# Kernel optimization log

Hardware: AMD Instinct MI355X
Metric: run time of the kernel (lower is better)

Reference implementation:

```python
import jax, jax.numpy as jnp
import numpy as np

RADIUS = 1.0
NSAMPLE = 32


def setup_inputs() -> dict:
    key = jax.random.key(0)
    k1, k2, k3, k4, k5 = jax.random.split(key, 5)
    B, Nb, M, K, C = 2, 2048, 64, 216, 32
    N = B * Nb
    # points in a 20m cube
    xyz = jax.random.uniform(k1, (N, 3), dtype=jnp.float32) * 20.0
    xyz_batch_cnt = jnp.array([Nb, Nb], dtype=jnp.int32)
    # rois: [x,y,z,dx,dy,dz,ry]
    ctr = jax.random.uniform(k2, (B, M, 3), dtype=jnp.float32) * 20.0
    dims = 1.0 + jax.random.uniform(k3, (B, M, 3), dtype=jnp.float32) * 2.0
    ry = jax.random.uniform(k4, (B, M, 1), dtype=jnp.float32) * 6.28
    rois = jnp.concatenate([ctr, dims, ry], axis=-1)
    # 6x6x6 grid points jittered around each roi center
    off = (jax.random.uniform(k5, (B, M, K, 3), dtype=jnp.float32) - 0.5) * 3.0
    new_xyz = ctr[:, :, None, :] + off
    features = jax.random.normal(jax.random.fold_in(key, 7), (N, C), dtype=jnp.float32)
    return {"xyz": xyz, "xyz_batch_cnt": xyz_batch_cnt, "new_xyz": new_xyz,
            "rois": rois, "features": features}


def _query_and_group(xyz, new_xyz, rois, features, B, Nb):
    """Ball query -> ragged compaction (padded to L=N*nsample) -> gather."""
    M, K = new_xyz.shape[1], new_xyz.shape[2]
    MK = M * K
    N = B * Nb
    L = N * NSAMPLE
    xyz_b = xyz.reshape(B, Nb, 3)
    grid = new_xyz.reshape(B, MK, 3)
    # squared distances point -> grid center, (B, Nb, MK)
    d2 = jnp.sum((xyz_b[:, :, None, :] - grid[:, None, :, :]) ** 2, axis=-1)
    # roi bounding sphere: center rois[:,:,:3], radius ||dims||_2 (the `ball` tensor)
    ctr = rois[:, :, :3]
    r2 = jnp.sum(rois[:, :, 3:6] ** 2, axis=-1)          # (B, M)
    d2b = jnp.sum((xyz_b[:, :, None, :] - ctr[:, None, :, :]) ** 2, axis=-1)  # (B,Nb,M)
    in_ball = (d2b <= r2[:, None, :])[:, :, :, None]      # (B,Nb,M,1)
    mask = (d2 <= RADIUS * RADIUS) & jnp.broadcast_to(in_ball, (B, Nb, M, K)).reshape(B, Nb, MK)
    # first-NSAMPLE-in-order selection per point (matches kernel iteration order)
    rank = jnp.cumsum(mask.astype(jnp.int32), axis=2) - 1
    cols = jnp.where(mask & (rank < NSAMPLE), rank, NSAMPLE)  # NSAMPLE = OOB -> dropped
    rows = jnp.broadcast_to(
        jnp.arange(B, dtype=jnp.int32)[:, None, None] * Nb
        + jnp.arange(Nb, dtype=jnp.int32)[None, :, None], (B, Nb, MK))
    flat_idx = jnp.broadcast_to(
        jnp.arange(B, dtype=jnp.int32)[:, None, None] * MK
        + jnp.arange(MK, dtype=jnp.int32)[None, None, :], (B, Nb, MK))
    ball_idx = jnp.full((N, NSAMPLE), -1, dtype=jnp.int32)
    ball_idx = ball_idx.at[rows.reshape(-1), cols.reshape(-1)].set(
        flat_idx.reshape(-1), mode="drop")
    # BallIndice: cumsum compaction of valid (point_idx, grid_idx) pairs, row-major
    valid = (ball_idx > -1).reshape(-1)                  # (L,)
    pos = jnp.cumsum(valid.astype(jnp.int32)) - 1
    pos_w = jnp.where(valid, pos, L)                     # invalid -> OOB -> dropped
    row_ids = jnp.broadcast_to(
        jnp.arange(N, dtype=jnp.int32)[:, None], (N, NSAMPLE)).reshape(-1)
    set_indices = jnp.zeros((L,), jnp.int32).at[pos_w].set(row_ids, mode="drop")
    set_new_indices = jnp.zeros((L,), jnp.int32).at[pos_w].set(
        ball_idx.reshape(-1), mode="drop")
    nind = jnp.sum(valid.astype(jnp.int32))
    vm = (jnp.arange(L) < nind)[:, None].astype(features.dtype)  # padding mask
    # GatherFeature (padded slots zeroed, matching new_zeros semantics)
    group_xyz = xyz[set_indices] * vm
    group_new_xyz = new_xyz.reshape(-1, 3)[set_new_indices] * vm
    group_feat = features[set_indices] * vm
    group_features = jnp.concatenate([group_xyz - group_new_xyz, group_feat], axis=1)
    return group_features, set_new_indices


def reference(xyz, xyz_batch_cnt, new_xyz, rois, features):
    B = xyz_batch_cnt.shape[0]
    Nb = xyz.shape[0] // B
    return _query_and_group(xyz, new_xyz, rois, features, B, Nb)
```

## Files before the change

### kernel.cpp

```cpp
#include <hip/hip_runtime.h>


#pragma clang fp contract(off)

typedef unsigned long long u64;

#define MAXN 4096

__global__ __launch_bounds__(256) void count_kernel(
    const float* __restrict__ xyz, const float* __restrict__ new_xyz,
    const float* __restrict__ rois, int* __restrict__ counts,
    int* __restrict__ blockSums, int* __restrict__ ballidx,
    int N, int Nb, int M, int K, int nsample)
{
    __shared__ int plist[4][64];
    __shared__ int scnt[4];
    const int wave = threadIdx.x >> 6;
    const int lane = threadIdx.x & 63;
    const int r = blockIdx.x * 4 + wave;
    const u64 laneLt = (1ull << lane) - 1ull;

    int cntc = 0;
    if (r < N) {
        const int b  = r / Nb;
        const float px = xyz[3 * r + 0];
        const float py = xyz[3 * r + 1];
        const float pz = xyz[3 * r + 2];

        bool pass = false;
        if (lane < M) {
            const float* rp = rois + (size_t)(b * M + lane) * 7;
            const float dx = rp[3], dy = rp[4], dz = rp[5];
            const float r2 = (dx * dx + dy * dy) + dz * dz;
            const float ex = px - rp[0], ey = py - rp[1], ez = pz - rp[2];
            pass = ((ex * ex + ey * ey) + ez * ez) <= r2;
        }
        const u64 roiMask = __ballot(pass);
        if (roiMask) {
            if (pass) plist[wave][__popcll(roiMask & laneLt)] = lane;

            const int P = __popcll(roiMask);
            const int total = P * K;
            const float* nb_ = new_xyz + (size_t)(b * M * K) * 3;
            int* bi = ballidx + (size_t)r * nsample;

            int cnt = 0;
            for (int base = 0; base < total && cnt < nsample; base += 512) {
                bool match[8];
                int jj[8];
                #pragma unroll
                for (int u = 0; u < 8; u++) {
                    const int p = base + u * 64 + lane;
                    match[u] = false; jj[u] = 0;
                    if (p < total) {
                        const int ri = p / K;
                        const int k  = p - ri * K;
                        const int j  = plist[wave][ri] * K + k;
                        jj[u] = j;
                        const float* gp = nb_ + (size_t)j * 3;
                        const float ax = px - gp[0], ay = py - gp[1], az = pz - gp[2];
                        match[u] = ((ax * ax + ay * ay) + az * az) <= 1.0f;
                    }
                }
                #pragma unroll
                for (int u = 0; u < 8; u++) {
                    const u64 mm = __ballot(match[u]);
                    const int slot = cnt + __popcll(mm & laneLt);
                    if (match[u] && slot < nsample) bi[slot] = jj[u];
                    cnt += __popcll(mm);
                }
            }
            cntc = cnt > nsample ? nsample : cnt;
        }
        if (lane == 0) counts[r] = cntc;
    }
    if (lane == 0) scnt[wave] = cntc;
    __syncthreads();
    if (threadIdx.x == 0)
        blockSums[blockIdx.x] = scnt[0] + scnt[1] + scnt[2] + scnt[3];
}

__global__ __launch_bounds__(256) void emit_kernel(
    const float* __restrict__ xyz, const float* __restrict__ new_xyz,
    const float* __restrict__ features,
    const int* __restrict__ counts, const int* __restrict__ blockSums,
    const int* __restrict__ ballidx,
    float* __restrict__ out_feat, float* __restrict__ out_idx,
    int N, int Nb, int M, int K, int C, int nsample, int numBlocks)
{
    __shared__ int sred[8];
    const int t = threadIdx.x;
    const int lane = t & 63;
    const int wid = t >> 6;
    const int bid = blockIdx.x;

    int pre = 0, tot = 0;
    {
        const int g = (t + bid) & 255;
        const int b0 = g * 4;
        #pragma unroll
        for (int i = 0; i < 4; i++) {
            const int bb = b0 + i;
            if (bb < numBlocks) {
                const int v = blockSums[bb];
                tot += v;
                if (bb < bid) pre += v;
            }
        }
        #pragma unroll
        for (int d = 1; d < 64; d <<= 1) {
            pre += __shfl_xor(pre, d, 64);
            tot += __shfl_xor(tot, d, 64);
        }
        if (lane == 0) { sred[wid] = pre; sred[4 + wid] = tot; }
    }
    __syncthreads();
    const int blockPre = sred[0] + sred[1] + sred[2] + sred[3];
    const int nind     = sred[4] + sred[5] + sred[6] + sred[7];

    const int W = 3 + C;
    const size_t L = (size_t)N * nsample;
    const int r0 = bid * 4;
    const int r  = r0 + wid;

    if (r < N) {
        const int cnt = counts[r];
        if (cnt > 0) {
            int rowpre = 0;
            if (lane < wid && (r0 + lane) < N) rowpre = counts[r0 + lane];
            #pragma unroll
            for (int d = 1; d < 64; d <<= 1) rowpre += __shfl_xor(rowpre, d, 64);

            const int b  = r / Nb;
            const int MK = M * K;
            const int obase = blockPre + rowpre;
            const int* bi = ballidx + (size_t)r * nsample;
            const float px = xyz[3 * r + 0];
            const float py = xyz[3 * r + 1];
            const float pz = xyz[3 * r + 2];
            const float* fr = features + (size_t)r * C;
            const float* nb_ = new_xyz + (size_t)b * MK * 3;

            float* dst = out_feat + (size_t)obase * W;
            const int totE = cnt * W;
            for (int idx = lane; idx < totE; idx += 64) {
                const int s = idx / W;
                const int c = idx - s * W;
                const int j = bi[s];
                float v;
                if (c == 0)      v = px - nb_[(size_t)j * 3 + 0];
                else if (c == 1) v = py - nb_[(size_t)j * 3 + 1];
                else if (c == 2) v = pz - nb_[(size_t)j * 3 + 2];
                else             v = fr[c - 3];
                dst[idx] = v;
            }
            for (int s = lane; s < cnt; s += 64)
                out_idx[obase + s] = (float)(b * MK + bi[s]);
        }
    }

    const int gtid = bid * 256 + t;
    const int gthreads = gridDim.x * 256;
    {
        const size_t sA = (size_t)nind * W;
        const size_t eA = L * (size_t)W;
        if (sA < eA) {
            const size_t s4 = (sA + 3) & ~(size_t)3;
            const size_t headEnd = s4 < eA ? s4 : eA;
            if ((size_t)gtid < headEnd - sA) out_feat[sA + gtid] = 0.0f;
            if (s4 < eA) {
                const size_t nvec = (eA - s4) >> 2;
                float4* p4 = (float4*)(out_feat + s4);
                const float4 z = make_float4(0.0f, 0.0f, 0.0f, 0.0f);
                for (size_t i = gtid; i < nvec; i += gthreads) p4[i] = z;
                const size_t rem = (eA - s4) & 3;
                if ((size_t)gtid < rem) out_feat[eA - rem + gtid] = 0.0f;
            }
        }
    }
    for (size_t i = (size_t)nind + gtid; i < L; i += gthreads)
        out_idx[i] = 0.0f;
}

extern "C" void kernel_launch(void* const* d_in, const int* in_sizes, int n_in,
                              void* d_out, int out_size, void* d_ws, size_t ws_size,
                              hipStream_t stream) {
    if (n_in < 5) return;

    int bc = 0;
    for (int i = 1; i < n_in; i++) if (in_sizes[i] < in_sizes[bc]) bc = i;
    const int B = in_sizes[bc];
    if (B < 1) return;

    int xi = -1, nwi = -1, ri = -1, fi = -1;
    int N = 0, M = 0, K = 0, C = 0, nsample = 0;

    for (int rr = 0; rr < n_in && xi < 0; rr++) {
        if (rr == bc) continue;
        if (in_sizes[rr] % (7 * B)) continue;
        const int M_ = in_sizes[rr] / (7 * B);
        if (M_ < 1 || M_ > 64) continue;
        for (int xx = 0; xx < n_in && xi < 0; xx++) {
            if (xx == bc || xx == rr) continue;
            if (in_sizes[xx] % 3) continue;
            const int N_ = in_sizes[xx] / 3;
            if (N_ < B || N_ % B || N_ > MAXN) continue;
            for (int nn = 0; nn < n_in && xi < 0; nn++) {
                if (nn == bc || nn == rr || nn == xx) continue;
                if (in_sizes[nn] % (3 * B * M_)) continue;
                const int K_ = in_sizes[nn] / (3 * B * M_);
                if (K_ < 1) continue;
                for (int ff = 0; ff < n_in && xi < 0; ff++) {
                    if (ff == bc || ff == rr || ff == xx || ff == nn) continue;
                    if (in_sizes[ff] % N_) continue;
                    const int C_ = in_sizes[ff] / N_;
                    if (C_ < 1) continue;
                    if (out_size % (4 + C_)) continue;
                    const long long L_ = (long long)out_size / (4 + C_);
                    if (L_ % N_) continue;
                    const int ns = (int)(L_ / N_);
                    if (ns < 1 || ns > 1024) continue;
                    xi = xx; nwi = nn; ri = rr; fi = ff;
                    N = N_; M = M_; K = K_; C = C_; nsample = ns;
                }
            }
        }
    }
    if (xi < 0) return;

    const float* xyz      = (const float*)d_in[xi];
    const float* new_xyz  = (const float*)d_in[nwi];
    const float* rois     = (const float*)d_in[ri];
    const float* features = (const float*)d_in[fi];
    const int Nb = N / B;

    const size_t L      = (size_t)N * nsample;
    const size_t chunk0 = L * (size_t)(3 + C);

    float* out_feat = (float*)d_out;
    float* out_idx  = out_feat + chunk0;

    const int blocks = (N + 3) / 4;

    const size_t wsNeed = ((size_t)N + (size_t)blocks + (size_t)N * nsample) * sizeof(int);
    if (ws_size < wsNeed) return;
    int* counts    = (int*)d_ws;
    int* blockSums = counts + N;
    int* ballidx   = blockSums + blocks;

    count_kernel<<<blocks, 256, 0, stream>>>(
        xyz, new_xyz, rois, counts, blockSums, ballidx,
        N, Nb, M, K, nsample);
    emit_kernel<<<blocks, 256, 0, stream>>>(
        xyz, new_xyz, features, counts, blockSums, ballidx,
        out_feat, out_idx, N, Nb, M, K, C, nsample, blocks);
}
```

Baseline: 88.35 us.

## Use 8 rows per block, 16-bit ball indices, nontemporal stores, per-wave prefix

Block size doubles to 512 threads with 8 rows per block, which halves the grid. Ball indices are stored as 16-bit values when M*K fits, shrinking the workspace traffic. Every output write, including the large zero-fill, now uses a nontemporal store to avoid cache pollution. The block prefix sum is computed redundantly in each wave over all block sums, dropping the shared-memory reduction and the barrier, but each wave now loops over more entries.

New measurement: 90.41 us. 1.02x slower.

```diff
diff --git a/kernel.cpp b/kernel.cpp
--- a/kernel.cpp
+++ b/kernel.cpp
@@ -4,20 +4,23 @@
 #pragma clang fp contract(off)
 
 typedef unsigned long long u64;
+typedef float f32x4 __attribute__((ext_vector_type(4)));
 
 #define MAXN 4096
-
-__global__ __launch_bounds__(256) void count_kernel(
+#define RPB 8
+
+template <typename IT>
+__global__ __launch_bounds__(512) void count_kernel(
     const float* __restrict__ xyz, const float* __restrict__ new_xyz,
     const float* __restrict__ rois, int* __restrict__ counts,
-    int* __restrict__ blockSums, int* __restrict__ ballidx,
+    int* __restrict__ blockSums, IT* __restrict__ ballidx,
     int N, int Nb, int M, int K, int nsample)
 {
-    __shared__ int plist[4][64];
-    __shared__ int scnt[4];
+    __shared__ int plist[RPB][64];
+    __shared__ int scnt[RPB];
     const int wave = threadIdx.x >> 6;
     const int lane = threadIdx.x & 63;
-    const int r = blockIdx.x * 4 + wave;
+    const int r = blockIdx.x * RPB + wave;
     const u64 laneLt = (1ull << lane) - 1ull;
 
     int cntc = 0;
@@ -42,7 +45,7 @@
             const int P = __popcll(roiMask);
             const int total = P * K;
             const float* nb_ = new_xyz + (size_t)(b * M * K) * 3;
-            int* bi = ballidx + (size_t)r * nsample;
+            IT* bi = ballidx + (size_t)r * nsample;
 
             int cnt = 0;
             for (int base = 0; base < total && cnt < nsample; base += 512) {
@@ -66,7 +69,7 @@
                 for (int u = 0; u < 8; u++) {
                     const u64 mm = __ballot(match[u]);
                     const int slot = cnt + __popcll(mm & laneLt);
-                    if (match[u] && slot < nsample) bi[slot] = jj[u];
+                    if (match[u] && slot < nsample) bi[slot] = (IT)jj[u];
                     cnt += __popcll(mm);
                 }
             }
@@ -76,19 +79,23 @@
     }
     if (lane == 0) scnt[wave] = cntc;
     __syncthreads();
-    if (threadIdx.x == 0)
-        blockSums[blockIdx.x] = scnt[0] + scnt[1] + scnt[2] + scnt[3];
+    if (threadIdx.x == 0) {
+        int s = 0;
+        #pragma unroll
+        for (int i = 0; i < RPB; i++) s += scnt[i];
+        blockSums[blockIdx.x] = s;
+    }
 }
 
-__global__ __launch_bounds__(256) void emit_kernel(
+template <typename IT>
+__global__ __launch_bounds__(512) void emit_kernel(
     const float* __restrict__ xyz, const float* __restrict__ new_xyz,
     const float* __restrict__ features,
     const int* __restrict__ counts, const int* __restrict__ blockSums,
-    const int* __restrict__ ballidx,
+    const IT* __restrict__ ballidx,
     float* __restrict__ out_feat, float* __restrict__ out_idx,
     int N, int Nb, int M, int K, int C, int nsample, int numBlocks)
 {
-    __shared__ int sred[8];
     const int t = threadIdx.x;
     const int lane = t & 63;
     const int wid = t >> 6;
@@ -96,31 +103,24 @@
 
     int pre = 0, tot = 0;
     {
-        const int g = (t + bid) & 255;
-        const int b0 = g * 4;
-        #pragma unroll
-        for (int i = 0; i < 4; i++) {
-            const int bb = b0 + i;
-            if (bb < numBlocks) {
-                const int v = blockSums[bb];
-                tot += v;
-                if (bb < bid) pre += v;
-            }
+        const int g = (lane + bid) & 63;
+        for (int idx = g; idx < numBlocks; idx += 64) {
+            const int v = blockSums[idx];
+            tot += v;
+            if (idx < bid) pre += v;
         }
         #pragma unroll
         for (int d = 1; d < 64; d <<= 1) {
             pre += __shfl_xor(pre, d, 64);
             tot += __shfl_xor(tot, d, 64);
         }
-        if (lane == 0) { sred[wid] = pre; sred[4 + wid] = tot; }
-    }
-    __syncthreads();
-    const int blockPre = sred[0] + sred[1] + sred[2] + sred[3];
-    const int nind     = sred[4] + sred[5] + sred[6] + sred[7];
+    }
+    const int blockPre = pre;
+    const int nind     = tot;
 
     const int W = 3 + C;
     const size_t L = (size_t)N * nsample;
-    const int r0 = bid * 4;
+    const int r0 = bid * RPB;
     const int r  = r0 + wid;
 
     if (r < N) {
@@ -134,7 +134,7 @@
             const int b  = r / Nb;
             const int MK = M * K;
             const int obase = blockPre + rowpre;
-            const int* bi = ballidx + (size_t)r * nsample;
+            const IT* bi = ballidx + (size_t)r * nsample;
             const float px = xyz[3 * r + 0];
             const float py = xyz[3 * r + 1];
             const float pz = xyz[3 * r + 2];
@@ -146,40 +146,44 @@
             for (int idx = lane; idx < totE; idx += 64) {
                 const int s = idx / W;
                 const int c = idx - s * W;
-                const int j = bi[s];
+                const int j = (int)bi[s];
                 float v;
                 if (c == 0)      v = px - nb_[(size_t)j * 3 + 0];
                 else if (c == 1) v = py - nb_[(size_t)j * 3 + 1];
                 else if (c == 2) v = pz - nb_[(size_t)j * 3 + 2];
                 else             v = fr[c - 3];
-                dst[idx] = v;
+                __builtin_nontemporal_store(v, &dst[idx]);
             }
             for (int s = lane; s < cnt; s += 64)
-                out_idx[obase + s] = (float)(b * MK + bi[s]);
-        }
-    }
-
-    const int gtid = bid * 256 + t;
-    const int gthreads = gridDim.x * 256;
+                __builtin_nontemporal_store((float)(b * MK + (int)bi[s]),
+                                            &out_idx[obase + s]);
+        }
+    }
+
+    const int gtid = bid * 512 + t;
+    const size_t gthreads = (size_t)numBlocks * 512;
     {
         const size_t sA = (size_t)nind * W;
         const size_t eA = L * (size_t)W;
         if (sA < eA) {
             const size_t s4 = (sA + 3) & ~(size_t)3;
             const size_t headEnd = s4 < eA ? s4 : eA;
-            if ((size_t)gtid < headEnd - sA) out_feat[sA + gtid] = 0.0f;
+            if ((size_t)gtid < headEnd - sA)
+                __builtin_nontemporal_store(0.0f, &out_feat[sA + gtid]);
             if (s4 < eA) {
                 const size_t nvec = (eA - s4) >> 2;
-                float4* p4 = (float4*)(out_feat + s4);
-                const float4 z = make_float4(0.0f, 0.0f, 0.0f, 0.0f);
-                for (size_t i = gtid; i < nvec; i += gthreads) p4[i] = z;
+                f32x4* p4 = (f32x4*)(out_feat + s4);
+                const f32x4 z = {0.0f, 0.0f, 0.0f, 0.0f};
+                for (size_t i = gtid; i < nvec; i += gthreads)
+                    __builtin_nontemporal_store(z, &p4[i]);
                 const size_t rem = (eA - s4) & 3;
-                if ((size_t)gtid < rem) out_feat[eA - rem + gtid] = 0.0f;
+                if ((size_t)gtid < rem)
+                    __builtin_nontemporal_store(0.0f, &out_feat[eA - rem + gtid]);
             }
         }
     }
     for (size_t i = (size_t)nind + gtid; i < L; i += gthreads)
-        out_idx[i] = 0.0f;
+        __builtin_nontemporal_store(0.0f, &out_idx[i]);
 }
 
 extern "C" void kernel_launch(void* const* d_in, const int* in_sizes, int n_in,
@@ -240,18 +244,29 @@
     float* out_feat = (float*)d_out;
     float* out_idx  = out_feat + chunk0;
 
-    const int blocks = (N + 3) / 4;
+    const int blocks = (N + RPB - 1) / RPB;
 
     const size_t wsNeed = ((size_t)N + (size_t)blocks + (size_t)N * nsample) * sizeof(int);
     if (ws_size < wsNeed) return;
     int* counts    = (int*)d_ws;
     int* blockSums = counts + N;
-    int* ballidx   = blockSums + blocks;
-
-    count_kernel<<<blocks, 256, 0, stream>>>(
-        xyz, new_xyz, rois, counts, blockSums, ballidx,
-        N, Nb, M, K, nsample);
-    emit_kernel<<<blocks, 256, 0, stream>>>(
-        xyz, new_xyz, features, counts, blockSums, ballidx,
-        out_feat, out_idx, N, Nb, M, K, C, nsample, blocks);
+    void* ballidx  = (void*)(blockSums + blocks);
+
+    const bool idx16 = ((long long)M * K <= 65535);
+
+    if (idx16) {
+        count_kernel<unsigned short><<<blocks, 512, 0, stream>>>(
+            xyz, new_xyz, rois, counts, blockSums, (unsigned short*)ballidx,
+            N, Nb, M, K, nsample);
+        emit_kernel<unsigned short><<<blocks, 512, 0, stream>>>(
+            xyz, new_xyz, features, counts, blockSums, (const unsigned short*)ballidx,
+            out_feat, out_idx, N, Nb, M, K, C, nsample, blocks);
+    } else {
+        count_kernel<int><<<blocks, 512, 0, stream>>>(
+            xyz, new_xyz, rois, counts, blockSums, (int*)ballidx,
+            N, Nb, M, K, nsample);
+        emit_kernel<int><<<blocks, 512, 0, stream>>>(
+            xyz, new_xyz, features, counts, blockSums, (const int*)ballidx,
+            out_feat, out_idx, N, Nb, M, K, C, nsample, blocks);
+    }
 }
```
